# Kernel optimization log

Measured on AMD Instinct MI355X. Metric: run time of the kernel, lower is better.

## Reference

```python
import jax, jax.numpy as jnp
import numpy as np

B = 128; NMAX = 128; H = 1024; HH = 256; NZ = 64; M = 20; LAT = 128; NCLS = 10; SD = 5
IN_DIM = SD + NCLS + LAT  # 143


def setup_inputs() -> dict:
    key = jax.random.key(0)
    ks = jax.random.split(key, 24)
    r = lambda i, shape, s=0.05: jax.random.normal(ks[i], shape, dtype=jnp.float32) * s
    cls_idx = jax.random.randint(ks[20], (B,), 0, NCLS)
    return dict(
        z=jax.random.normal(ks[0], (B, LAT), dtype=jnp.float32),
        classifier=jax.nn.one_hot(cls_idx, NCLS, dtype=jnp.float32),
        fc_in_W=r(1, (2 * H + 2 * HH, LAT)),
        fc_in_b=jnp.zeros((2 * H + 2 * HH,), jnp.float32),
        Wx=r(2, (4 * H, IN_DIM)),
        Wh=r(3, (4 * H, H)),
        b0=jnp.zeros((4, H), jnp.float32),
        hWx=r(4, (4 * HH, IN_DIM + H)),
        hWh=r(5, (4 * HH, HH)),
        hb=jnp.zeros((4 * HH,), jnp.float32),
        Whz_x=r(6, (4 * NZ, HH)),
        Whz_h=r(7, (4 * NZ, HH)),
        Whz_b=r(8, (4 * NZ, HH)),
        Wdz_x=r(9, (4, H, NZ), 0.1),
        Wdz_h=r(10, (4, H, NZ), 0.1),
        Wdz_b=r(11, (4, H, NZ), 0.1),
        proj_W=r(12, (6 * M + 3, H)),
        proj_b=jnp.zeros((6 * M + 3,), jnp.float32),
        eps=jax.random.normal(ks[13], (NMAX, B, 2), dtype=jnp.float32),
        umix=jax.random.uniform(ks[14], (NMAX, B, M), dtype=jnp.float32),
        upen=jax.random.uniform(ks[15], (NMAX, B, 3), dtype=jnp.float32),
    )


def _gumbel(u):
    u = jnp.clip(u, 1e-7, 1.0 - 1e-7)
    return -jnp.log(-jnp.log(u))


def reference(z, classifier, fc_in_W, fc_in_b, Wx, Wh, b0, hWx, hWh, hb,
              Whz_x, Whz_h, Whz_b, Wdz_x, Wdz_h, Wdz_b, proj_W, proj_b,
              eps, umix, upen):
    sig = jax.nn.sigmoid
    # initial states: tanh(fc_in(z)) split into h, c, h_hat, c_hat
    s = jnp.tanh(z @ fc_in_W.T + fc_in_b)
    h0 = s[:, :H]; c0 = s[:, H:2 * H]
    hh0 = s[:, 2 * H:2 * H + HH]; ch0 = s[:, 2 * H + HH:]
    prev0 = jnp.tile(jnp.array([0., 0., 1., 0., 0.], jnp.float32), (B, 1))
    empty = jnp.array([0., 0., 0., 0., 1.], jnp.float32)

    def mod(hh, Whz, Wdz):
        zg = (hh @ Whz.T).reshape(B, 4, NZ)          # hyper embedding per gate
        return jnp.einsum('bkz,khz->bkh', zg, Wdz)   # [B,4,H] gate scalings

    def step(carry, xs):
        prev, h, c, hh, ch = carry
        eps_t, um_t, up_t = xs
        x = jnp.concatenate([prev, classifier, z], axis=1)    # [B, IN_DIM]
        # hyper LSTM step on [x, h]
        hx = jnp.concatenate([x, h], axis=1)
        g4 = hx @ hWx.T + hh @ hWh.T + hb                     # [B, 4*HH]
        hi, hf, hg, ho = jnp.split(g4, 4, axis=1)
        ch_n = sig(hf) * ch + sig(hi) * jnp.tanh(hg)
        hh_n = sig(ho) * jnp.tanh(ch_n)
        # main LSTM gates modulated by hyper outputs
        dX = mod(hh_n, Whz_x, Wdz_x)
        dH = mod(hh_n, Whz_h, Wdz_h)
        dB = mod(hh_n, Whz_b, Wdz_b)
        gx = (x @ Wx.T).reshape(B, 4, H)
        gh = (h @ Wh.T).reshape(B, 4, H)
        pre = dX * gx + dH * gh + dB + b0                     # [B,4,H]
        i_, f_, g_, o_ = pre[:, 0], pre[:, 1], pre[:, 2], pre[:, 3]
        c_n = sig(f_) * c + sig(i_) * jnp.tanh(g_)
        h_n = sig(o_) * jnp.tanh(c_n)
        # MDN params + sampling
        y = h_n @ proj_W.T + proj_b                           # [B, 6M+3]
        pi_h = y[:, :M]
        mux = y[:, M:2 * M]; muy = y[:, 2 * M:3 * M]
        sxh = y[:, 3 * M:4 * M]; syh = y[:, 4 * M:5 * M]
        rhoh = y[:, 5 * M:6 * M]; pen = y[:, 6 * M:]
        k = jnp.argmax(jax.nn.log_softmax(pi_h) + _gumbel(um_t), axis=1)
        take = lambda a: jnp.take_along_axis(a, k[:, None], axis=1)[:, 0]
        mx, my = take(mux), take(muy)
        sx, sy = jnp.exp(take(sxh)), jnp.exp(take(syh))
        rho = jnp.tanh(take(rhoh))
        dx_s = mx + sx * eps_t[:, 0]
        dy_s = my + sy * (rho * eps_t[:, 0] + jnp.sqrt(1.0 - rho ** 2) * eps_t[:, 1])
        pidx = jnp.argmax(jax.nn.log_softmax(pen) + _gumbel(up_t), axis=1)
        pen_oh = jax.nn.one_hot(pidx, 3, dtype=y.dtype)
        stroke = jnp.concatenate([dx_s[:, None], dy_s[:, None], pen_oh], axis=1)
        done = pen_oh[:, 2:3] > 0.5                           # p3==1 -> empty stroke
        stroke = jnp.where(done, empty, stroke)
        return (stroke, h_n, c_n, hh_n, ch_n), stroke

    _, strokes = jax.lax.scan(jax.checkpoint(step), (prev0, h0, c0, hh0, ch0),
                              (eps, umix, upen))
    return strokes  # [NMAX, B, 5]
```

## Files before the change

kernel.cpp:

```cpp
#include <hip/hip_runtime.h>
#include <hip/hip_cooperative_groups.h>

namespace cg = cooperative_groups;

#define NBLK 256
#define NTHR 512

constexpr int WS_H    = 0;
constexpr int WS_HHS  = 131072;
constexpr int WS_Y    = 163840;
constexpr int WS_WEFF = 180224;
constexpr int WS_BAR  = WS_WEFF + 256*12288;

__device__ __forceinline__ float dot4(float4 a, float4 b){
  return a.x*b.x + a.y*b.y + a.z*b.z + a.w*b.w;
}
__device__ __forceinline__ float sigf(float x){ return 1.0f/(1.0f + expf(-x)); }
__device__ __forceinline__ float gumb(float u){
  u = fminf(fmaxf(u, 1e-7f), 1.0f - 1e-7f);
  return -logf(-logf(u));
}

__device__ __forceinline__ void st_cg(float* p, float v){
  asm volatile("global_store_dword %0, %1, off sc0 sc1" :: "v"(p), "v"(v) : "memory");
}

__device__ __forceinline__ void gridbar(unsigned* barc, unsigned n){
  asm volatile("s_waitcnt vmcnt(0)" ::: "memory");
  __syncthreads();
  if (threadIdx.x == 0){
    const unsigned g = blockIdx.x >> 5;
    unsigned old = __hip_atomic_fetch_add(barc + 32 + g*32, 1u,
                     __ATOMIC_RELAXED, __HIP_MEMORY_SCOPE_AGENT);
    if (old + 1 == n*32)
      __hip_atomic_fetch_add(barc, 1u, __ATOMIC_RELAXED, __HIP_MEMORY_SCOPE_AGENT);
    while (__hip_atomic_load(barc, __ATOMIC_RELAXED, __HIP_MEMORY_SCOPE_AGENT) < n*8)
      __builtin_amdgcn_s_sleep(1);
  }
  __syncthreads();
  __builtin_amdgcn_fence(__ATOMIC_ACQUIRE, "agent");
}

extern "C" __global__ void __launch_bounds__(NTHR, 2)
vae_kernel(const float* __restrict__ z,     const float* __restrict__ cls,
           const float* __restrict__ fcW,   const float* __restrict__ fcb,
           const float* __restrict__ Wx,    const float* __restrict__ Wh,
           const float* __restrict__ bias0, const float* __restrict__ hWx,
           const float* __restrict__ hWh,   const float* __restrict__ hb,
           const float* __restrict__ Whz_x, const float* __restrict__ Whz_h,
           const float* __restrict__ Whz_b, const float* __restrict__ Wdz_x,
           const float* __restrict__ Wdz_h, const float* __restrict__ Wdz_b,
           const float* __restrict__ projW, const float* __restrict__ projb,
           const float* __restrict__ eps_,  const float* __restrict__ umix,
           const float* __restrict__ upen,
           float* __restrict__ out, float* __restrict__ ws)
{
  cg::grid_group grid = cg::this_grid();
  const int tid = threadIdx.x;
  const int bid = blockIdx.x;
  const int l = tid & 63;
  const int w = tid >> 6;
  const int rq = w & 3;
  const int bh = w >> 2;

  float* hws   = ws + WS_H;
  float* hhws  = ws + WS_HHS;
  float* yws   = ws + WS_Y;
  float* weffw = ws + WS_WEFF;
  unsigned* barc = (unsigned*)(ws + WS_BAR);

  __shared__ __align__(16) float lds_h[16896];
  __shared__ __align__(16) float lds_GH[2176];
  __shared__ __align__(16) float lds_Gp[640];
  __shared__ __align__(16) float lds_prev[1152];
  __shared__ __align__(16) float lds_gmix[2688];
  __shared__ __align__(16) float lds_gpen[640];
  __shared__ float lds_wxp[80];
  __shared__ float lds_hwxp[20];
  __shared__ float lds_b0[16];

  if (bid == 0 && tid < 9){
    unsigned* p = (tid == 0) ? barc : (barc + 32 + (tid-1)*32);
    __hip_atomic_store(p, 0u, __ATOMIC_RELAXED, __HIP_MEMORY_SCOPE_AGENT);
  }

  float4 wWh[4][4];
  #pragma unroll
  for (int j = 0; j < 4; ++j){
    const int row = rq*1024 + bid*4 + j;
    #pragma unroll
    for (int m = 0; m < 4; ++m)
      wWh[j][m] = *((const float4*)(Wh + ((size_t)row << 10) + m*256) + l);
  }
  float4 wHx[4];
  {
    const int row = rq*256 + bid;
    #pragma unroll
    for (int m = 0; m < 4; ++m){
      const float* s = hWx + (size_t)row*1167 + 143 + m*256 + l*4;
      wHx[m] = make_float4(s[0], s[1], s[2], s[3]);
    }
  }
  float4 wHh = *((const float4*)(hWh + ((size_t)(rq*256 + bid) << 8)) + l);

  const bool isproj = (bid >= 128 && bid < 251);
  const int prow = bid - 128;
  float4 wPj[4] = {make_float4(0,0,0,0),make_float4(0,0,0,0),make_float4(0,0,0,0),make_float4(0,0,0,0)};
  float pjb = 0.f;
  if (isproj){
    #pragma unroll
    for (int m = 0; m < 4; ++m)
      wPj[m] = *((const float4*)(projW + ((size_t)prow << 10) + m*256) + l);
    pjb = projb[prow];
  }

  const int eb = tid >> 2, ej = tid & 3;
  float cgxr[4];
  #pragma unroll
  for (int k = 0; k < 4; ++k){
    const float* wr = Wx + (size_t)(k*1024 + bid*4 + ej)*143;
    float a = 0.f;
    for (int n = 0; n < 10; ++n) a += cls[eb*10+n]*wr[5+n];
    const float* zr = z + (eb << 7);
    #pragma unroll 8
    for (int i = 0; i < 128; ++i) a += zr[i]*wr[15+i];
    cgxr[k] = a;
  }
  float cst;
  {
    int col = 1024 + bid*4 + ej;
    float a = fcb[col];
    const float* wr = fcW + (col << 7);
    const float* zr = z + (eb << 7);
    #pragma unroll 8
    for (int i = 0; i < 128; ++i) a += zr[i]*wr[i];
    cst = tanhf(a);
  }
  {
    int col = bid*4 + ej;
    float a = fcb[col];
    const float* wr = fcW + (col << 7);
    const float* zr = z + (eb << 7);
    #pragma unroll 8
    for (int i = 0; i < 128; ++i) a += zr[i]*wr[i];
    st_cg(&hws[(eb << 10) + col], tanhf(a));
  }
  float cg4r[4] = {0,0,0,0};
  float chst = 0.f;
  if (tid < 128){
    int b = tid;
    const float* zr = z + (b << 7);
    #pragma unroll
    for (int gi = 0; gi < 4; ++gi){
      int row = gi*256 + bid;
      const float* wr = hWx + (size_t)row*1167;
      float a = hb[row];
      for (int n = 0; n < 10; ++n) a += cls[b*10+n]*wr[5+n];
      #pragma unroll 8
      for (int i = 0; i < 128; ++i) a += zr[i]*wr[15+i];
      cg4r[gi] = a;
    }
    {
      int col = 2304 + bid;
      float a = fcb[col];
      const float* wr = fcW + (col << 7);
      #pragma unroll 8
      for (int i = 0; i < 128; ++i) a += zr[i]*wr[i];
      chst = tanhf(a);
    }
    {
      int col = 2048 + bid;
      float a = fcb[col];
      const float* wr = fcW + (col << 7);
      #pragma unroll 8
      for (int i = 0; i < 128; ++i) a += zr[i]*wr[i];
      st_cg(&hhws[(b << 8) + bid], tanhf(a));
    }
    lds_prev[tid*9+0] = 0.f; lds_prev[tid*9+1] = 0.f; lds_prev[tid*9+2] = 1.f;
    lds_prev[tid*9+3] = 0.f; lds_prev[tid*9+4] = 0.f;
  }
  if (tid < 80){
    int r16 = tid/5, p = tid - r16*5;
    lds_wxp[tid] = Wx[(size_t)((r16>>2)*1024 + bid*4 + (r16&3))*143 + p];
  }
  if (tid < 20){
    int gi = tid/5, p = tid - gi*5;
    lds_hwxp[tid] = hWx[(size_t)(gi*256 + bid)*1167 + p];
  }
  if (tid < 16) lds_b0[tid] = bias0[(tid>>2)*1024 + bid*4 + (tid&3)];

  {
    const float* Wdzp[3] = {Wdz_x, Wdz_h, Wdz_b};
    const float* Whzp[3] = {Whz_x, Whz_h, Whz_b};
    for (int n = 0; n < 24; ++n){
      int gidx = tid + 512*n;
      int m = gidx >> 12, rem = gidx & 4095;
      int r = rem >> 8, c = rem & 255;
      int k = r >> 2, j = r & 3;
      const float* wd = Wdzp[m] + (size_t)(k*1024 + bid*4 + j)*64;
      const float* wzb = Whzp[m] + c;
      float a = 0.f;
      #pragma unroll 8
      for (int zz = 0; zz < 64; ++zz) a += wd[zz]*wzb[(k*64+zz) << 8];
      weffw[(size_t)bid*12288 + gidx] = a;
    }
  }
  grid.sync();

  unsigned barno = 0;
  float4 wf[12];

  auto p1_comp = [&](float4 a0, float4 a1, float4 a2, float4 a3, float4 hv, int b){
    float acc[4];
    #pragma unroll
    for (int j = 0; j < 4; ++j)
      acc[j] = dot4(a0,wWh[j][0]) + dot4(a1,wWh[j][1])
             + dot4(a2,wWh[j][2]) + dot4(a3,wWh[j][3]);
    float gac = dot4(a0,wHx[0]) + dot4(a1,wHx[1]) + dot4(a2,wHx[2]) + dot4(a3,wHx[3])
              + dot4(hv, wHh);
    const bool b5 = (l & 32), b4 = (l & 16);
    #pragma unroll
    for (int q = 0; q < 2; ++q){
      float snd = b5 ? acc[q] : acc[q+2];
      float rcv = __shfl_xor(snd, 32, 64);
      acc[q] = (b5 ? acc[q+2] : acc[q]) + rcv;
    }
    {
      float snd = b4 ? acc[0] : acc[1];
      float rcv = __shfl_xor(snd, 16, 64);
      float s = (b4 ? acc[1] : acc[0]) + rcv;
      s += __shfl_xor(s, 8, 64);
      s += __shfl_xor(s, 4, 64);
      s += __shfl_xor(s, 2, 64);
      s += __shfl_xor(s, 1, 64);
      if ((l & 15) == 0)
        lds_GH[b*17 + rq*4 + (b5 ? 2 : 0) + (b4 ? 1 : 0)] = s;
    }
    {
      float s = gac;
      s += __shfl_xor(s, 32, 64);
      s += __shfl_xor(s, 16, 64);
      s += __shfl_xor(s, 8, 64);
      s += __shfl_xor(s, 4, 64);
      s += __shfl_xor(s, 2, 64);
      s += __shfl_xor(s, 1, 64);
      if (l == 0) lds_Gp[b*5 + rq] = s;
    }
    if (isproj && ((b & 3) == rq)){
      float ya = dot4(a0,wPj[0]) + dot4(a1,wPj[1]) + dot4(a2,wPj[2]) + dot4(a3,wPj[3]);
      ya += __shfl_xor(ya, 32, 64);
      ya += __shfl_xor(ya, 16, 64);
      ya += __shfl_xor(ya, 8, 64);
      ya += __shfl_xor(ya, 4, 64);
      ya += __shfl_xor(ya, 2, 64);
      ya += __shfl_xor(ya, 1, 64);
      if (l == 0) st_cg(&yws[(b << 7) + prow], ya + pjb);
    }
  };

  for (int t = 0; t <= 128; ++t){
    {
      const float4* hb4  = (const float4*)hws;
      const float4* hhb4 = (const float4*)hhws;
      const int bq = bh*64;
      float4 A0,A1,A2,A3,AH, B0,B1,B2,B3,BH;
      {
        const float4* hp = hb4 + ((size_t)bq << 8);
        A0 = hp[l]; A1 = hp[64+l]; A2 = hp[128+l]; A3 = hp[192+l];
        AH = hhb4[(bq << 6) + l];
        const float4* hp2 = hb4 + ((size_t)(bq+1) << 8);
        B0 = hp2[l]; B1 = hp2[64+l]; B2 = hp2[128+l]; B3 = hp2[192+l];
        BH = hhb4[((bq+1) << 6) + l];
      }
      for (int it = 0; it < 64; it += 2){
        p1_comp(A0,A1,A2,A3,AH, bq+it);
        if (it < 62){
          const float4* hp = hb4 + ((size_t)(bq+it+2) << 8);
          A0 = hp[l]; A1 = hp[64+l]; A2 = hp[128+l]; A3 = hp[192+l];
          AH = hhb4[((bq+it+2) << 6) + l];
        }
        p1_comp(B0,B1,B2,B3,BH, bq+it+1);
        if (it < 62){
          const float4* hp = hb4 + ((size_t)(bq+it+3) << 8);
          B0 = hp[l]; B1 = hp[64+l]; B2 = hp[128+l]; B3 = hp[192+l];
          BH = hhb4[((bq+it+3) << 6) + l];
        }
      }
    }
    gridbar(barc, ++barno);

    #pragma unroll
    for (int m = 0; m < 3; ++m)
      #pragma unroll
      for (int j = 0; j < 4; ++j)
        wf[m*4+j] = *((const float4*)(weffw + (size_t)bid*12288 + m*4096 + ((rq*4+j) << 8)) + l);

    if (t >= 1){
      {
        const float4* ysrc = (const float4*)yws;
        float4 q[8];
        #pragma unroll
        for (int k = 0; k < 8; ++k) q[k] = ysrc[(tid>>2)*32 + (tid&3)*8 + k];
        float4* dst = (float4*)(lds_h + (tid>>2)*132 + (tid&3)*32);
        #pragma unroll
        for (int k = 0; k < 8; ++k) dst[k] = q[k];
      }
      if (tid >= 128){
        const int i0 = tid - 128;
        for (int i = i0; i < 2560; i += 384){
          int bb = i/20, mm = i - bb*20;
          lds_gmix[bb*21+mm] = gumb(umix[(t-1)*2560 + i]);
        }
        { int bb = i0/3, pp = i0 - bb*3;
          lds_gpen[bb*5+pp] = gumb(upen[(t-1)*384 + i0]); }
      }
      __syncthreads();
      if (tid < 128){
        const int b = tid;
        const float* yb = lds_h + b*132;
        int km = 0; float best = -1e30f;
        for (int m = 0; m < 20; ++m){
          float v = yb[m] + lds_gmix[b*21+m];
          if (v > best){ best = v; km = m; }
        }
        const float mx = yb[20+km], my = yb[40+km];
        const float sx = expf(yb[60+km]), sy = expf(yb[80+km]);
        const float rho = tanhf(yb[100+km]);
        const float e0 = eps_[((t-1)*128 + b)*2 + 0], e1 = eps_[((t-1)*128 + b)*2 + 1];
        const float dxs = mx + sx*e0;
        const float dys = my + sy*(rho*e0 + sqrtf(1.0f - rho*rho)*e1);
        int pp = 0; best = -1e30f;
        for (int p = 0; p < 3; ++p){
          float v = yb[120+p] + lds_gpen[b*5+p];
          if (v > best){ best = v; pp = p; }
        }
        float s0,s1,s2,s3,s4;
        if (pp == 2){ s0=0.f; s1=0.f; s2=0.f; s3=0.f; s4=1.f; }
        else { s0=dxs; s1=dys; s2=(pp==0)?1.f:0.f; s3=(pp==1)?1.f:0.f; s4=0.f; }
        if (bid == 0){
          float* o = out + ((t-1)*128 + b)*5;
          st_cg(o+0, s0); st_cg(o+1, s1); st_cg(o+2, s2); st_cg(o+3, s3); st_cg(o+4, s4);
        }
        lds_prev[b*9+0]=s0; lds_prev[b*9+1]=s1; lds_prev[b*9+2]=s2;
        lds_prev[b*9+3]=s3; lds_prev[b*9+4]=s4;
      }
    }
    if (t == 128) break;
    if (tid < 128){
      const int b = tid;
      const float pv0 = lds_prev[b*9+0], pv1 = lds_prev[b*9+1], pv2 = lds_prev[b*9+2],
                  pv3 = lds_prev[b*9+3], pv4 = lds_prev[b*9+4];
      float gv[4];
      #pragma unroll
      for (int gi = 0; gi < 4; ++gi)
        gv[gi] = lds_Gp[b*5 + gi] + cg4r[gi]
               + pv0*lds_hwxp[gi*5+0] + pv1*lds_hwxp[gi*5+1] + pv2*lds_hwxp[gi*5+2]
               + pv3*lds_hwxp[gi*5+3] + pv4*lds_hwxp[gi*5+4];
      const float chn = sigf(gv[1])*chst + sigf(gv[0])*tanhf(gv[2]);
      chst = chn;
      const float hhn = sigf(gv[3])*tanhf(chn);
      st_cg(&hhws[(b << 8) + bid], hhn);
    }
    gridbar(barc, ++barno);

    {
      float* lds_scr = lds_h;
      const float4* hq = (const float4*)hhws;
      const int b0 = bh*64;
      float4 pf[4];
      #pragma unroll
      for (int i = 0; i < 4; ++i) pf[i] = hq[(b0 + i)*64 + l];
      #pragma unroll 4
      for (int it = 0; it < 64; ++it){
        const float4 ch = pf[it & 3];
        if (it < 60) pf[it & 3] = hq[(b0 + it + 4)*64 + l];
        const int b = b0 + it;
        float v[12];
        #pragma unroll
        for (int q = 0; q < 12; ++q) v[q] = dot4(ch, wf[q]);
        {
          const bool b5 = (l & 32), b4 = (l & 16), b3 = (l & 8);
          #pragma unroll
          for (int q = 0; q < 6; ++q){
            float snd = b5 ? v[q] : v[q+6];
            float rcv = __shfl_xor(snd, 32, 64);
            v[q] = (b5 ? v[q+6] : v[q]) + rcv;
          }
          #pragma unroll
          for (int q = 0; q < 3; ++q){
            float snd = b4 ? v[q] : v[q+3];
            float rcv = __shfl_xor(snd, 16, 64);
            v[q] = (b4 ? v[q+3] : v[q]) + rcv;
          }
          float snd = b3 ? v[0] : v[1];
          float rcv = __shfl_xor(snd, 8, 64);
          float ab = (b3 ? v[1] : v[0]) + rcv;
          ab += __shfl_xor(ab, 4, 64);
          ab += __shfl_xor(ab, 2, 64);
          ab += __shfl_xor(ab, 1, 64);
          float c2 = v[2];
          c2 += __shfl_xor(c2, 8, 64);
          c2 += __shfl_xor(c2, 4, 64);
          c2 += __shfl_xor(c2, 2, 64);
          c2 += __shfl_xor(c2, 1, 64);
          const int base = (b5 ? 6 : 0) + (b4 ? 3 : 0);
          if ((l & 15) == 0){
            lds_scr[b*50 + rq*12 + base + 0] = ab;
            lds_scr[b*50 + rq*12 + base + 2] = c2;
          } else if ((l & 15) == 8){
            lds_scr[b*50 + rq*12 + base + 1] = ab;
          }
        }
      }
      __syncthreads();
      {
        float pv[5];
        #pragma unroll
        for (int p = 0; p < 5; ++p) pv[p] = lds_prev[eb*9 + p];
        float pre[4];
        #pragma unroll
        for (int k = 0; k < 4; ++k){
          const float dXv = lds_scr[eb*50 + k*12 + ej];
          const float dHv = lds_scr[eb*50 + k*12 + 4 + ej];
          const float dBv = lds_scr[eb*50 + k*12 + 8 + ej];
          float gxv = cgxr[k];
          #pragma unroll
          for (int p = 0; p < 5; ++p) gxv += pv[p]*lds_wxp[(k*4+ej)*5 + p];
          pre[k] = dXv*gxv + dHv*lds_GH[eb*17 + k*4 + ej] + dBv + lds_b0[k*4+ej];
        }
        const float cn = sigf(pre[1])*cst + sigf(pre[0])*tanhf(pre[2]);
        cst = cn;
        const float hn = sigf(pre[3])*tanhf(cn);
        st_cg(&hws[(eb << 10) + bid*4 + ej], hn);
      }
    }
    gridbar(barc, ++barno);
  }
}

extern "C" void kernel_launch(void* const* d_in, const int* in_sizes, int n_in,
                              void* d_out, int out_size, void* d_ws, size_t ws_size,
                              hipStream_t stream)
{
  const float* z     = (const float*)d_in[0];
  const float* cls   = (const float*)d_in[1];
  const float* fcW   = (const float*)d_in[2];
  const float* fcb   = (const float*)d_in[3];
  const float* Wx    = (const float*)d_in[4];
  const float* Wh    = (const float*)d_in[5];
  const float* bias0 = (const float*)d_in[6];
  const float* hWx   = (const float*)d_in[7];
  const float* hWh   = (const float*)d_in[8];
  const float* hb    = (const float*)d_in[9];
  const float* Whz_x = (const float*)d_in[10];
  const float* Whz_h = (const float*)d_in[11];
  const float* Whz_b = (const float*)d_in[12];
  const float* Wdz_x = (const float*)d_in[13];
  const float* Wdz_h = (const float*)d_in[14];
  const float* Wdz_b = (const float*)d_in[15];
  const float* projW = (const float*)d_in[16];
  const float* projb = (const float*)d_in[17];
  const float* eps_  = (const float*)d_in[18];
  const float* umix  = (const float*)d_in[19];
  const float* upen  = (const float*)d_in[20];
  float* out = (float*)d_out;
  float* ws  = (float*)d_ws;

  void* args[] = { (void*)&z, (void*)&cls, (void*)&fcW, (void*)&fcb, (void*)&Wx, (void*)&Wh,
                   (void*)&bias0, (void*)&hWx, (void*)&hWh, (void*)&hb,
                   (void*)&Whz_x, (void*)&Whz_h, (void*)&Whz_b,
                   (void*)&Wdz_x, (void*)&Wdz_h, (void*)&Wdz_b,
                   (void*)&projW, (void*)&projb, (void*)&eps_, (void*)&umix, (void*)&upen,
                   (void*)&out, (void*)&ws };
  (void)hipLaunchCooperativeKernel((const void*)vae_kernel, dim3(NBLK), dim3(NTHR), args, 0, stream);
}
```

Measured before the change: 19.49 ms.

## Merge gate reductions, deepen prefetch, and parallelize sampling across all threads

Folds the separate hyper-gate wavefront reduction into the main gate butterfly, sharing the xor-8 stage and dropping several shuffles per batch row. Raises the prefetch depth of h rows in phase 1 to four and of hyper-h rows in the later phase to eight, to hide more global-load latency. Spreads the mixture and pen sampling across four threads per batch row, with the Gumbel noise computed in registers and reduced by shuffle argmax, instead of 128 threads scanning serially; this removes the LDS Gumbel buffers. The deeper prefetch raises register pressure and adds an extra __syncthreads per step, and the tie-breaking rule in the argmax has to match the serial version.

New measurement: 25.41 ms. 1.3x slower.

```diff
diff --git a/kernel.cpp b/kernel.cpp
--- a/kernel.cpp
+++ b/kernel.cpp
@@ -73,8 +73,6 @@
   __shared__ __align__(16) float lds_GH[2176];
   __shared__ __align__(16) float lds_Gp[640];
   __shared__ __align__(16) float lds_prev[1152];
-  __shared__ __align__(16) float lds_gmix[2688];
-  __shared__ __align__(16) float lds_gpen[640];
   __shared__ float lds_wxp[80];
   __shared__ float lds_hwxp[20];
   __shared__ float lds_b0[16];
@@ -218,33 +216,31 @@
              + dot4(a2,wWh[j][2]) + dot4(a3,wWh[j][3]);
     float gac = dot4(a0,wHx[0]) + dot4(a1,wHx[1]) + dot4(a2,wHx[2]) + dot4(a3,wHx[3])
               + dot4(hv, wHh);
-    const bool b5 = (l & 32), b4 = (l & 16);
+    const bool b5 = (l & 32), b4 = (l & 16), b3 = (l & 8);
     #pragma unroll
     for (int q = 0; q < 2; ++q){
       float snd = b5 ? acc[q] : acc[q+2];
       float rcv = __shfl_xor(snd, 32, 64);
       acc[q] = (b5 ? acc[q+2] : acc[q]) + rcv;
     }
+    gac += __shfl_xor(gac, 32, 64);
     {
       float snd = b4 ? acc[0] : acc[1];
       float rcv = __shfl_xor(snd, 16, 64);
-      float s = (b4 ? acc[1] : acc[0]) + rcv;
-      s += __shfl_xor(s, 8, 64);
+      acc[0] = (b4 ? acc[1] : acc[0]) + rcv;
+    }
+    gac += __shfl_xor(gac, 16, 64);
+    {
+      float snd = b3 ? acc[0] : gac;
+      float rcv = __shfl_xor(snd, 8, 64);
+      float s = (b3 ? gac : acc[0]) + rcv;
       s += __shfl_xor(s, 4, 64);
       s += __shfl_xor(s, 2, 64);
       s += __shfl_xor(s, 1, 64);
       if ((l & 15) == 0)
         lds_GH[b*17 + rq*4 + (b5 ? 2 : 0) + (b4 ? 1 : 0)] = s;
-    }
-    {
-      float s = gac;
-      s += __shfl_xor(s, 32, 64);
-      s += __shfl_xor(s, 16, 64);
-      s += __shfl_xor(s, 8, 64);
-      s += __shfl_xor(s, 4, 64);
-      s += __shfl_xor(s, 2, 64);
-      s += __shfl_xor(s, 1, 64);
-      if (l == 0) lds_Gp[b*5 + rq] = s;
+      else if (l == 8)
+        lds_Gp[b*5 + rq] = s;
     }
     if (isproj && ((b & 3) == rq)){
       float ya = dot4(a0,wPj[0]) + dot4(a1,wPj[1]) + dot4(a2,wPj[2]) + dot4(a3,wPj[3]);
@@ -263,28 +259,23 @@
       const float4* hb4  = (const float4*)hws;
       const float4* hhb4 = (const float4*)hhws;
       const int bq = bh*64;
-      float4 A0,A1,A2,A3,AH, B0,B1,B2,B3,BH;
-      {
-        const float4* hp = hb4 + ((size_t)bq << 8);
-        A0 = hp[l]; A1 = hp[64+l]; A2 = hp[128+l]; A3 = hp[192+l];
-        AH = hhb4[(bq << 6) + l];
-        const float4* hp2 = hb4 + ((size_t)(bq+1) << 8);
-        B0 = hp2[l]; B1 = hp2[64+l]; B2 = hp2[128+l]; B3 = hp2[192+l];
-        BH = hhb4[((bq+1) << 6) + l];
-      }
-      for (int it = 0; it < 64; it += 2){
-        p1_comp(A0,A1,A2,A3,AH, bq+it);
-        if (it < 62){
-          const float4* hp = hb4 + ((size_t)(bq+it+2) << 8);
-          A0 = hp[l]; A1 = hp[64+l]; A2 = hp[128+l]; A3 = hp[192+l];
-          AH = hhb4[((bq+it+2) << 6) + l];
+      float4 P[4][5];
+      #pragma unroll
+      for (int i = 0; i < 4; ++i){
+        const float4* hp = hb4 + ((size_t)(bq+i) << 8);
+        P[i][0] = hp[l]; P[i][1] = hp[64+l]; P[i][2] = hp[128+l]; P[i][3] = hp[192+l];
+        P[i][4] = hhb4[((bq+i) << 6) + l];
+      }
+      #pragma unroll 4
+      for (int it = 0; it < 64; ++it){
+        const float4 a0 = P[it&3][0], a1 = P[it&3][1], a2 = P[it&3][2],
+                     a3 = P[it&3][3], hv = P[it&3][4];
+        if (it < 60){
+          const float4* hp = hb4 + ((size_t)(bq+it+4) << 8);
+          P[it&3][0] = hp[l]; P[it&3][1] = hp[64+l]; P[it&3][2] = hp[128+l]; P[it&3][3] = hp[192+l];
+          P[it&3][4] = hhb4[((bq+it+4) << 6) + l];
         }
-        p1_comp(B0,B1,B2,B3,BH, bq+it+1);
-        if (it < 62){
-          const float4* hp = hb4 + ((size_t)(bq+it+3) << 8);
-          B0 = hp[l]; B1 = hp[64+l]; B2 = hp[128+l]; B3 = hp[192+l];
-          BH = hhb4[((bq+it+3) << 6) + l];
-        }
+        p1_comp(a0,a1,a2,a3,hv, bq+it);
       }
     }
     gridbar(barc, ++barno);
@@ -298,52 +289,59 @@
     if (t >= 1){
       {
         const float4* ysrc = (const float4*)yws;
-        float4 q[8];
+        float4 q4[8];
         #pragma unroll
-        for (int k = 0; k < 8; ++k) q[k] = ysrc[(tid>>2)*32 + (tid&3)*8 + k];
+        for (int k = 0; k < 8; ++k) q4[k] = ysrc[(tid>>2)*32 + (tid&3)*8 + k];
         float4* dst = (float4*)(lds_h + (tid>>2)*132 + (tid&3)*32);
         #pragma unroll
-        for (int k = 0; k < 8; ++k) dst[k] = q[k];
-      }
-      if (tid >= 128){
-        const int i0 = tid - 128;
-        for (int i = i0; i < 2560; i += 384){
-          int bb = i/20, mm = i - bb*20;
-          lds_gmix[bb*21+mm] = gumb(umix[(t-1)*2560 + i]);
-        }
-        { int bb = i0/3, pp = i0 - bb*3;
-          lds_gpen[bb*5+pp] = gumb(upen[(t-1)*384 + i0]); }
-      }
+        for (int k = 0; k < 8; ++k) dst[k] = q4[k];
+      }
+      const int sb = tid >> 2, sq = tid & 3;
+      float gm[5];
+      #pragma unroll
+      for (int i = 0; i < 5; ++i) gm[i] = gumb(umix[((t-1)*128 + sb)*20 + sq*5 + i]);
+      const float gpe = (sq < 3) ? gumb(upen[((t-1)*128 + sb)*3 + sq]) : -1e30f;
+      const float e0 = eps_[((t-1)*128 + sb)*2 + 0];
+      const float e1 = eps_[((t-1)*128 + sb)*2 + 1];
       __syncthreads();
-      if (tid < 128){
-        const int b = tid;
-        const float* yb = lds_h + b*132;
-        int km = 0; float best = -1e30f;
-        for (int m = 0; m < 20; ++m){
-          float v = yb[m] + lds_gmix[b*21+m];
-          if (v > best){ best = v; km = m; }
-        }
+      const float* yb = lds_h + sb*132;
+      float best = -1e30f; int km = 0;
+      #pragma unroll
+      for (int i = 0; i < 5; ++i){
+        float v = yb[sq*5+i] + gm[i];
+        if (v > best){ best = v; km = sq*5+i; }
+      }
+      #pragma unroll
+      for (int d = 1; d <= 2; d <<= 1){
+        float ov = __shfl_xor(best, d, 64);
+        int   oi = __shfl_xor(km,   d, 64);
+        if (ov > best || (ov == best && oi < km)){ best = ov; km = oi; }
+      }
+      float pbv = (sq < 3) ? yb[120+sq] + gpe : -1e30f;
+      int pbi = sq;
+      #pragma unroll
+      for (int d = 1; d <= 2; d <<= 1){
+        float ov = __shfl_xor(pbv, d, 64);
+        int   oi = __shfl_xor(pbi, d, 64);
+        if (ov > pbv || (ov == pbv && oi < pbi)){ pbv = ov; pbi = oi; }
+      }
+      if (sq == 0){
         const float mx = yb[20+km], my = yb[40+km];
         const float sx = expf(yb[60+km]), sy = expf(yb[80+km]);
         const float rho = tanhf(yb[100+km]);
-        const float e0 = eps_[((t-1)*128 + b)*2 + 0], e1 = eps_[((t-1)*128 + b)*2 + 1];
         const float dxs = mx + sx*e0;
         const float dys = my + sy*(rho*e0 + sqrtf(1.0f - rho*rho)*e1);
-        int pp = 0; best = -1e30f;
-        for (int p = 0; p < 3; ++p){
-          float v = yb[120+p] + lds_gpen[b*5+p];
-          if (v > best){ best = v; pp = p; }
-        }
         float s0,s1,s2,s3,s4;
-        if (pp == 2){ s0=0.f; s1=0.f; s2=0.f; s3=0.f; s4=1.f; }
-        else { s0=dxs; s1=dys; s2=(pp==0)?1.f:0.f; s3=(pp==1)?1.f:0.f; s4=0.f; }
+        if (pbi == 2){ s0=0.f; s1=0.f; s2=0.f; s3=0.f; s4=1.f; }
+        else { s0=dxs; s1=dys; s2=(pbi==0)?1.f:0.f; s3=(pbi==1)?1.f:0.f; s4=0.f; }
         if (bid == 0){
-          float* o = out + ((t-1)*128 + b)*5;
+          float* o = out + ((t-1)*128 + sb)*5;
           st_cg(o+0, s0); st_cg(o+1, s1); st_cg(o+2, s2); st_cg(o+3, s3); st_cg(o+4, s4);
         }
-        lds_prev[b*9+0]=s0; lds_prev[b*9+1]=s1; lds_prev[b*9+2]=s2;
-        lds_prev[b*9+3]=s3; lds_prev[b*9+4]=s4;
-      }
+        lds_prev[sb*9+0]=s0; lds_prev[sb*9+1]=s1; lds_prev[sb*9+2]=s2;
+        lds_prev[sb*9+3]=s3; lds_prev[sb*9+4]=s4;
+      }
+      __syncthreads();
     }
     if (t == 128) break;
     if (tid < 128){
@@ -367,13 +365,13 @@
       float* lds_scr = lds_h;
       const float4* hq = (const float4*)hhws;
       const int b0 = bh*64;
-      float4 pf[4];
-      #pragma unroll
-      for (int i = 0; i < 4; ++i) pf[i] = hq[(b0 + i)*64 + l];
-      #pragma unroll 4
+      float4 pf[8];
+      #pragma unroll
+      for (int i = 0; i < 8; ++i) pf[i] = hq[(b0 + i)*64 + l];
+      #pragma unroll 8
       for (int it = 0; it < 64; ++it){
-        const float4 ch = pf[it & 3];
-        if (it < 60) pf[it & 3] = hq[(b0 + it + 4)*64 + l];
+        const float4 ch = pf[it & 7];
+        if (it < 56) pf[it & 7] = hq[(b0 + it + 8)*64 + l];
         const int b = b0 + it;
         float v[12];
         #pragma unroll
```
